# Kernel tuning notes

Hardware: AMD Instinct MI355X
Metric: run time of the kernel (lower is better)

## Reference

```python
import jax, jax.numpy as jnp
import numpy as np

D_MODEL, D_STATE, D_CONV, EXPAND = 32, 64, 4, 2
D_INNER = EXPAND * D_MODEL  # 64 == D_STATE, required by the bmm in the torch source
B, H, W = 4, 48, 48


def setup_inputs() -> dict:
    key = jax.random.key(0)
    ks = jax.random.split(key, 8)
    s = lambda k, sh, sc: jax.random.normal(k, sh, jnp.float32) * sc
    return {
        "x": s(ks[0], (B, H, W, D_MODEL), 1.0),
        "W_in": s(ks[1], (2 * D_INNER, D_MODEL), 0.1),
        "conv_w": s(ks[2], (D_INNER, D_CONV), 0.3),   # depthwise kernel [d_inner, k]
        "conv_b": jnp.zeros((D_INNER,), jnp.float32),
        "W_x": s(ks[3], (D_STATE + 2 * D_INNER, D_INNER), 0.1),
        "W_dt": s(ks[4], (D_INNER, D_STATE), 0.1),
        "b_dt": jnp.zeros((D_INNER,), jnp.float32),
        "A_log": jnp.log(jnp.tile(jnp.arange(1, D_STATE + 1, dtype=jnp.float32), (D_INNER, 1))),
        "D": jnp.ones((D_INNER,), jnp.float32),
        "W_out": s(ks[5], (D_MODEL, D_INNER), 0.1),
    }


def _ssm(x, W_in, conv_w, conv_b, W_x, W_dt, b_dt, A_log, D, W_out):
    # x: [Bn, L, d_model]
    Bn, L, _ = x.shape
    xz = x @ W_in.T                                   # [Bn,L,2*di]
    x_ssm, z = jnp.split(xz, 2, axis=-1)
    # causal depthwise conv1d (pad left k-1, truncate to L)
    xp = jnp.pad(x_ssm, ((0, 0), (D_CONV - 1, 0), (0, 0)))
    xc = conv_b + sum(xp[:, k:k + L, :] * conv_w[:, k] for k in range(D_CONV))
    x_ssm = jax.nn.silu(xc)
    sp = x_ssm @ W_x.T                                # [Bn,L,ds+2*di]
    d_in, Bp, Cp = jnp.split(sp, [D_STATE, D_STATE + D_INNER], axis=-1)
    delta = jax.nn.softplus(d_in @ W_dt.T + b_dt)     # [Bn,L,di]
    A = -jnp.exp(A_log)                               # [di,ds]
    A_bar = jnp.exp(delta[..., None] * A)             # [Bn,L,di,ds]
    B_bar = delta * Bp                                # [Bn,L,di] (broadcast to ds in step)

    def step(h, inp):
        Ab, Bb, c = inp                               # [Bn,di,ds], [Bn,di], [Bn,ds]
        h = Ab * h + Bb[..., None]
        return h, jnp.einsum('bds,bs->bd', h, c)      # == torch.bmm(h, c[...,None])

    h0 = jnp.zeros((Bn, D_INNER, D_STATE), x.dtype)
    _, ys = jax.lax.scan(step, h0, (A_bar.transpose(1, 0, 2, 3),
                                    B_bar.transpose(1, 0, 2),
                                    Cp.transpose(1, 0, 2)))
    y = ys.transpose(1, 0, 2) + D * x_ssm             # skip connection
    y = y * jax.nn.silu(z)                            # gate
    return y @ W_out.T


def reference(x, W_in, conv_w, conv_b, W_x, W_dt, b_dt, A_log, D, W_out):
    p = (W_in, conv_w, conv_b, W_x, W_dt, b_dt, A_log, D, W_out)
    Bsz, Hh, Ww, C = x.shape
    ssm = lambda s: _ssm(s, *p)
    # horizontal scans: sequence along H, batch (b w)
    x_h = x.transpose(0, 2, 1, 3).reshape(Bsz * Ww, Hh, C)
    yh_f = ssm(x_h)
    yh_b = ssm(x_h[:, ::-1])[:, ::-1]
    back_h = lambda t: t.reshape(Bsz, Ww, Hh, C).transpose(0, 2, 1, 3)
    # vertical scans: sequence along W, batch (b h)
    x_v = x.reshape(Bsz * Hh, Ww, C)
    yv_f = ssm(x_v)
    yv_b = ssm(x_v[:, ::-1])[:, ::-1]
    back_v = lambda t: t.reshape(Bsz, Hh, Ww, C)
    return back_h(yh_f) + back_h(yh_b) + back_v(yv_f) + back_v(yv_b)
```

## Files before the change

kernel.cpp:

```cpp
#include <hip/hip_runtime.h>
#include <hip/hip_bf16.h>


constexpr int BN = 4, SL = 48;
constexpr int NPIX = BN * SL * SL;
constexpr int L = SL;
constexpr int NSEQ = BN * SL;
constexpr int NBLK = 4 * NSEQ;
constexpr int PIXPB = 16;
constexpr int NPWB = NPIX / PIXPB;
constexpr int NPREP = 56;
constexpr int NPREB = NPWB + NPREP;

__global__ __launch_bounds__(256) void k_pre(
    const float* __restrict__ x, const float* __restrict__ Win,
    const float* __restrict__ Wdt, const float* __restrict__ Wx,
    const float* __restrict__ Wout,
    float* __restrict__ xraw, float* __restrict__ slz,
    float* __restrict__ PMs, float* __restrict__ PB,
    float* __restrict__ PC, float* __restrict__ PO,
    float* __restrict__ out) {
  __shared__ float xf[PIXPB * 32];
  __shared__ float wt[32 * 129];
  int bid = blockIdx.x, tid = threadIdx.x;

  for (int e = bid * 256 + tid; e < NPIX * 32; e += NPREB * 256) out[e] = 0.f;

  if (bid < NPWB) {
    int pix0 = bid * PIXPB;
    for (int e = tid; e < PIXPB * 32; e += 256) xf[e] = x[pix0 * 32 + e];
    for (int e = tid; e < 4096; e += 256) {
      int j = e >> 5, k = e & 31;
      wt[k * 129 + j] = Win[e];
    }
    __syncthreads();
    int g = tid >> 6, lane = tid & 63;
    float s0[4] = {0.f, 0.f, 0.f, 0.f}, s1[4] = {0.f, 0.f, 0.f, 0.f};
    for (int k = 0; k < 32; ++k) {
      float w0 = wt[k * 129 + lane];
      float w1 = wt[k * 129 + 64 + lane];
      #pragma unroll
      for (int pp = 0; pp < 4; ++pp) {
        float xk = xf[(g * 4 + pp) * 32 + k];
        s0[pp] += w0 * xk;
        s1[pp] += w1 * xk;
      }
    }
    #pragma unroll
    for (int pp = 0; pp < 4; ++pp) {
      int pix = pix0 + g * 4 + pp;
      xraw[pix * 64 + lane] = s0[pp];
      float z = s1[pp];
      slz[pix * 64 + lane] = z / (1.f + __expf(-z));
    }
  } else {
    int e = (bid - NPWB) * 256 + tid;
    if (e < 4096) {
      int i = e >> 6, d = e & 63;
      float s = 0.f;
      #pragma unroll 8
      for (int t = 0; t < 64; ++t) s += Wdt[i * 64 + t] * Wx[t * 64 + d];
      PMs[((d >> 2) * 64 + i) * 4 + (d & 3)] = s;
    } else if (e < 8192) {
      int e2 = e - 4096; int k = e2 >> 6, r = e2 & 63;
      PB[((k >> 2) * 64 + r) * 4 + (k & 3)] = Wx[(64 + r) * 64 + k];
    } else if (e < 12288) {
      int e2 = e - 8192; int k = e2 >> 6, r = e2 & 63;
      PC[((k >> 2) * 64 + r) * 4 + (k & 3)] = Wx[(128 + r) * 64 + k];
    } else {
      int e2 = e - 12288; int c = e2 & 31, d = e2 >> 5;
      PO[((d >> 2) * 32 + c) * 4 + (d & 3)] = Wout[c * 64 + d];
    }
  }
}

__global__ __launch_bounds__(256) void k_scan(
    const float* __restrict__ xraw, const float* __restrict__ slz,
    const float* __restrict__ PMs, const float* __restrict__ PB,
    const float* __restrict__ PC, const float* __restrict__ PO,
    const float* __restrict__ convw, const float* __restrict__ convb,
    const float* __restrict__ bdt, const float* __restrict__ Alog,
    const float* __restrict__ Dv, float* __restrict__ out) {
  __shared__ float xs_s[L * 64];
  __shared__ float u_s[L * 192];

  int tid = threadIdx.x;
  int bid = blockIdx.x;
  int dir = bid / NSEQ;
  int seq = bid % NSEQ;
  int b = seq / SL, q = seq % SL;
  int pbase, pstride;
  if (dir == 0)      { pbase = (b * SL) * SL + q;           pstride = SL;  }
  else if (dir == 1) { pbase = (b * SL + SL - 1) * SL + q;  pstride = -SL; }
  else if (dir == 2) { pbase = (b * SL + q) * SL;           pstride = 1;   }
  else               { pbase = (b * SL + q) * SL + SL - 1;  pstride = -1;  }

  int wv = tid >> 6, lane = tid & 63;

  float* xr = u_s;
  for (int t = wv; t < L; t += 4)
    xr[t * 64 + lane] = xraw[(pbase + t * pstride) * 64 + lane];
  __syncthreads();

  for (int e = tid; e < L * 64; e += 256) {
    int t = e >> 6, d = e & 63;
    float4 cw = reinterpret_cast<const float4*>(convw)[d];
    float s = convb[d] + xr[t * 64 + d] * cw.w;
    if (t >= 1) s += xr[(t - 1) * 64 + d] * cw.z;
    if (t >= 2) s += xr[(t - 2) * 64 + d] * cw.y;
    if (t >= 3) s += xr[(t - 3) * 64 + d] * cw.x;
    xs_s[e] = s / (1.f + __expf(-s));
  }
  __syncthreads();

  {
    int tr = wv * 12;
    float aD[12], aB[12], aC[12];
    #pragma unroll
    for (int j = 0; j < 12; ++j) { aD[j] = 0.f; aB[j] = 0.f; aC[j] = 0.f; }
    const float4* pms = reinterpret_cast<const float4*>(PMs);
    const float4* pb  = reinterpret_cast<const float4*>(PB);
    const float4* pc  = reinterpret_cast<const float4*>(PC);
    for (int k4 = 0; k4 < 16; ++k4) {
      float4 wd = pms[k4 * 64 + lane];
      float4 wb = pb[k4 * 64 + lane];
      float4 wc = pc[k4 * 64 + lane];
      #pragma unroll
      for (int j = 0; j < 12; ++j) {
        float4 x4 = *reinterpret_cast<const float4*>(xs_s + (tr + j) * 64 + k4 * 4);
        aD[j] += wd.x * x4.x + wd.y * x4.y + wd.z * x4.z + wd.w * x4.w;
        aB[j] += wb.x * x4.x + wb.y * x4.y + wb.z * x4.z + wb.w * x4.w;
        aC[j] += wc.x * x4.x + wc.y * x4.y + wc.z * x4.z + wc.w * x4.w;
      }
    }
    float bdl = bdt[lane];
    #pragma unroll
    for (int j = 0; j < 12; ++j) {
      float s = aD[j] + bdl;
      s = (s > 15.f) ? s : __logf(1.f + __expf(s));
      u_s[(tr + j) * 192 + lane]       = s;
      u_s[(tr + j) * 192 + 64 + lane]  = aB[j];
      u_s[(tr + j) * 192 + 128 + lane] = aC[j];
    }
  }
  __syncthreads();

  {
    int d = tid >> 2, sg = tid & 3;
    float A_[16], h[16];
    #pragma unroll
    for (int j = 0; j < 16; ++j) {
      A_[j] = -__expf(Alog[d * 64 + sg * 16 + j]);
      h[j] = 0.f;
    }
    float Dd = Dv[d];
    for (int t = 0; t < L; ++t) {
      float dlt = u_s[t * 192 + d];
      float bb  = dlt * u_s[t * 192 + 64 + d];
      const float* cp = u_s + t * 192 + 128 + sg * 16;
      float part = 0.f;
      #pragma unroll
      for (int j = 0; j < 16; ++j) {
        float ab = __expf(dlt * A_[j]);
        h[j] = ab * h[j] + bb;
        part += h[j] * cp[j];
      }
      part += __shfl_xor(part, 1);
      part += __shfl_xor(part, 2);
      if (sg == 0) u_s[t * 192 + d] = part + Dd * xs_s[t * 64 + d];
    }
  }
  __syncthreads();

  for (int e = tid; e < L * 64; e += 256) {
    int t = e >> 6, d = e & 63;
    u_s[t * 192 + d] *= slz[(pbase + t * pstride) * 64 + d];
  }
  __syncthreads();

  for (int e = tid; e < L * 32; e += 256) {
    int t = e >> 5, c = e & 31;
    const float4* po = reinterpret_cast<const float4*>(PO);
    const float* yv = u_s + t * 192;
    float s = 0.f;
    #pragma unroll
    for (int d4 = 0; d4 < 16; ++d4) {
      float4 w = po[d4 * 32 + c];
      const float* yp = yv + d4 * 4;
      s += w.x * yp[0] + w.y * yp[1] + w.z * yp[2] + w.w * yp[3];
    }
    atomicAdd(&out[(pbase + t * pstride) * 32 + c], s);
  }
}

extern "C" void kernel_launch(void* const* d_in, const int* in_sizes, int n_in,
                              void* d_out, int out_size, void* d_ws, size_t ws_size,
                              hipStream_t stream) {
  const float* x     = (const float*)d_in[0];
  const float* Win   = (const float*)d_in[1];
  const float* convw = (const float*)d_in[2];
  const float* convb = (const float*)d_in[3];
  const float* Wx    = (const float*)d_in[4];
  const float* Wdt   = (const float*)d_in[5];
  const float* bdt   = (const float*)d_in[6];
  const float* Alog  = (const float*)d_in[7];
  const float* Dv    = (const float*)d_in[8];
  const float* Wout  = (const float*)d_in[9];

  float* xraw = (float*)d_ws;
  float* slz  = xraw + NPIX * 64;
  float* PMs  = slz + NPIX * 64;
  float* PB   = PMs + 4096;
  float* PC   = PB + 4096;
  float* PO   = PC + 4096;
  float* out  = (float*)d_out;

  k_pre<<<NPREB, 256, 0, stream>>>(x, Win, Wdt, Wx, Wout, xraw, slz,
                                   PMs, PB, PC, PO, out);
  k_scan<<<NBLK, 256, 0, stream>>>(xraw, slz, PMs, PB, PC, PO, convw, convb,
                                   bdt, Alog, Dv, out);
}
```

Before: 135.9 us.

## Use bf16 MFMA for B/C projections and geometric A_bar recurrence in scan

Moves the B and C projections (x_ssm @ W_x rows 64..191) from scalar fp32 FMAs onto bf16 MFMA 16x16x32 instructions. It packs the weights into fragment layout in the prep kernel and stores a swizzled bf16 copy of x_ssm in shared memory. The scan detects at runtime when A is an arithmetic progression per row and builds the 16 exp(delta*A) values from two exp2 calls plus multiplies, instead of 16 exps. Shared memory is reorganised into smaller bf16 buffers, and launch bounds request 4 blocks per CU. B and C are stored in bf16, which lowers precision in the recurrence.

New measurement: 124.2 us. 8.6% less time.

```diff
diff --git a/kernel.cpp b/kernel.cpp
--- a/kernel.cpp
+++ b/kernel.cpp
@@ -1,5 +1,6 @@
 #include <hip/hip_runtime.h>
 #include <hip/hip_bf16.h>
+#include <stdint.h>
 
 
 constexpr int BN = 4, SL = 48;
@@ -12,14 +13,23 @@
 constexpr int NPREP = 56;
 constexpr int NPREB = NPWB + NPREP;
 
+typedef __attribute__((ext_vector_type(8))) short short8;
+typedef __attribute__((ext_vector_type(4))) float f32x4;
+
+#define DEVINL __device__ __forceinline__
+DEVINL ushort f2b(float f) {
+  uint u = __float_as_uint(f);
+  return (ushort)((u + 0x7FFFu + ((u >> 16) & 1u)) >> 16);
+}
+DEVINL float b2f(ushort u) { return __uint_as_float(((uint)u) << 16); }
+
 __global__ __launch_bounds__(256) void k_pre(
     const float* __restrict__ x, const float* __restrict__ Win,
     const float* __restrict__ Wdt, const float* __restrict__ Wx,
     const float* __restrict__ Wout,
     float* __restrict__ xraw, float* __restrict__ slz,
-    float* __restrict__ PMs, float* __restrict__ PB,
-    float* __restrict__ PC, float* __restrict__ PO,
-    float* __restrict__ out) {
+    float* __restrict__ PMs, float* __restrict__ PO,
+    ushort* __restrict__ PW2, float* __restrict__ out) {
   __shared__ float xf[PIXPB * 32];
   __shared__ float wt[32 * 129];
   int bid = blockIdx.x, tid = threadIdx.x;
@@ -61,12 +71,12 @@
       #pragma unroll 8
       for (int t = 0; t < 64; ++t) s += Wdt[i * 64 + t] * Wx[t * 64 + d];
       PMs[((d >> 2) * 64 + i) * 4 + (d & 3)] = s;
-    } else if (e < 8192) {
-      int e2 = e - 4096; int k = e2 >> 6, r = e2 & 63;
-      PB[((k >> 2) * 64 + r) * 4 + (k & 3)] = Wx[(64 + r) * 64 + k];
     } else if (e < 12288) {
-      int e2 = e - 8192; int k = e2 >> 6, r = e2 & 63;
-      PC[((k >> 2) * 64 + r) * 4 + (k & 3)] = Wx[(128 + r) * 64 + k];
+      int e2 = e - 4096;
+      int j = e2 & 7, l = (e2 >> 3) & 63, ks = (e2 >> 9) & 1, nt = e2 >> 10;
+      int k = ks * 32 + ((l >> 4) * 8) + j;
+      int row = 64 + nt * 16 + (l & 15);
+      PW2[e2] = f2b(Wx[row * 64 + k]);
     } else {
       int e2 = e - 12288; int c = e2 & 31, d = e2 >> 5;
       PO[((d >> 2) * 32 + c) * 4 + (d & 3)] = Wout[c * 64 + d];
@@ -74,15 +84,17 @@
   }
 }
 
-__global__ __launch_bounds__(256) void k_scan(
+__global__ __launch_bounds__(256, 4) void k_scan(
     const float* __restrict__ xraw, const float* __restrict__ slz,
-    const float* __restrict__ PMs, const float* __restrict__ PB,
-    const float* __restrict__ PC, const float* __restrict__ PO,
+    const float* __restrict__ PMs, const ushort* __restrict__ PW2,
+    const float* __restrict__ PO,
     const float* __restrict__ convw, const float* __restrict__ convb,
     const float* __restrict__ bdt, const float* __restrict__ Alog,
     const float* __restrict__ Dv, float* __restrict__ out) {
-  __shared__ float xs_s[L * 64];
-  __shared__ float u_s[L * 192];
+  __shared__ float R1[L * 64];
+  __shared__ __align__(16) ushort R2u[L * 136];
+  __shared__ float R3[L * 64];
+  __shared__ __align__(16) ushort R4u[L * 64];
 
   int tid = threadIdx.x;
   int bid = blockIdx.x;
@@ -97,40 +109,35 @@
 
   int wv = tid >> 6, lane = tid & 63;
 
-  float* xr = u_s;
   for (int t = wv; t < L; t += 4)
-    xr[t * 64 + lane] = xraw[(pbase + t * pstride) * 64 + lane];
+    R1[t * 64 + lane] = xraw[(pbase + t * pstride) * 64 + lane];
   __syncthreads();
 
   for (int e = tid; e < L * 64; e += 256) {
     int t = e >> 6, d = e & 63;
     float4 cw = reinterpret_cast<const float4*>(convw)[d];
-    float s = convb[d] + xr[t * 64 + d] * cw.w;
-    if (t >= 1) s += xr[(t - 1) * 64 + d] * cw.z;
-    if (t >= 2) s += xr[(t - 2) * 64 + d] * cw.y;
-    if (t >= 3) s += xr[(t - 3) * 64 + d] * cw.x;
-    xs_s[e] = s / (1.f + __expf(-s));
+    float s = convb[d] + R1[t * 64 + d] * cw.w;
+    if (t >= 1) s += R1[(t - 1) * 64 + d] * cw.z;
+    if (t >= 2) s += R1[(t - 2) * 64 + d] * cw.y;
+    if (t >= 3) s += R1[(t - 3) * 64 + d] * cw.x;
+    float xs = s / (1.f + __expf(-s));
+    R3[t * 64 + d] = xs;
+    R4u[t * 64 + (d ^ ((t & 7) << 3))] = f2b(xs);
   }
   __syncthreads();
 
   {
     int tr = wv * 12;
-    float aD[12], aB[12], aC[12];
-    #pragma unroll
-    for (int j = 0; j < 12; ++j) { aD[j] = 0.f; aB[j] = 0.f; aC[j] = 0.f; }
+    float aD[12];
+    #pragma unroll
+    for (int j = 0; j < 12; ++j) aD[j] = 0.f;
     const float4* pms = reinterpret_cast<const float4*>(PMs);
-    const float4* pb  = reinterpret_cast<const float4*>(PB);
-    const float4* pc  = reinterpret_cast<const float4*>(PC);
     for (int k4 = 0; k4 < 16; ++k4) {
       float4 wd = pms[k4 * 64 + lane];
-      float4 wb = pb[k4 * 64 + lane];
-      float4 wc = pc[k4 * 64 + lane];
       #pragma unroll
       for (int j = 0; j < 12; ++j) {
-        float4 x4 = *reinterpret_cast<const float4*>(xs_s + (tr + j) * 64 + k4 * 4);
+        float4 x4 = *reinterpret_cast<const float4*>(&R3[(tr + j) * 64 + k4 * 4]);
         aD[j] += wd.x * x4.x + wd.y * x4.y + wd.z * x4.z + wd.w * x4.w;
-        aB[j] += wb.x * x4.x + wb.y * x4.y + wb.z * x4.z + wb.w * x4.w;
-        aC[j] += wc.x * x4.x + wc.y * x4.y + wc.z * x4.z + wc.w * x4.w;
       }
     }
     float bdl = bdt[lane];
@@ -138,50 +145,116 @@
     for (int j = 0; j < 12; ++j) {
       float s = aD[j] + bdl;
       s = (s > 15.f) ? s : __logf(1.f + __expf(s));
-      u_s[(tr + j) * 192 + lane]       = s;
-      u_s[(tr + j) * 192 + 64 + lane]  = aB[j];
-      u_s[(tr + j) * 192 + 128 + lane] = aC[j];
-    }
+      R1[(tr + j) * 64 + lane] = s;
+    }
+  }
+
+  {
+    short8 bfrag[2][2];
+    const short8* pw8 = reinterpret_cast<const short8*>(PW2);
+    #pragma unroll
+    for (int ntl = 0; ntl < 2; ++ntl)
+      #pragma unroll
+      for (int ks = 0; ks < 2; ++ks)
+        bfrag[ntl][ks] = pw8[((2 * wv + ntl) * 2 + ks) * 64 + lane];
+    f32x4 acc[3][2];
+    #pragma unroll
+    for (int mt = 0; mt < 3; ++mt)
+      #pragma unroll
+      for (int ntl = 0; ntl < 2; ++ntl)
+        acc[mt][ntl] = (f32x4){0.f, 0.f, 0.f, 0.f};
+    #pragma unroll
+    for (int mt = 0; mt < 3; ++mt) {
+      int row = mt * 16 + (lane & 15);
+      #pragma unroll
+      for (int ks = 0; ks < 2; ++ks) {
+        int within = (ks * 32 + ((lane >> 4) * 8)) ^ ((row & 7) << 3);
+        short8 af = *reinterpret_cast<const short8*>(&R4u[row * 64 + within]);
+        acc[mt][0] = __builtin_amdgcn_mfma_f32_16x16x32_bf16(af, bfrag[0][ks], acc[mt][0], 0, 0, 0);
+        acc[mt][1] = __builtin_amdgcn_mfma_f32_16x16x32_bf16(af, bfrag[1][ks], acc[mt][1], 0, 0, 0);
+      }
+    }
+    #pragma unroll
+    for (int mt = 0; mt < 3; ++mt)
+      #pragma unroll
+      for (int ntl = 0; ntl < 2; ++ntl)
+        #pragma unroll
+        for (int qq = 0; qq < 4; ++qq) {
+          int t = mt * 16 + (lane >> 4) * 4 + qq;
+          int rr = (2 * wv + ntl) * 16 + (lane & 15);
+          R2u[t * 136 + rr] = f2b(acc[mt][ntl][qq]);
+        }
   }
   __syncthreads();
 
   {
     int d = tid >> 2, sg = tid & 3;
-    float A_[16], h[16];
-    #pragma unroll
-    for (int j = 0; j < 16; ++j) {
-      A_[j] = -__expf(Alog[d * 64 + sg * 16 + j]);
-      h[j] = 0.f;
-    }
+    float A_[16];
+    #pragma unroll
+    for (int j = 0; j < 16; ++j) A_[j] = -__expf(Alog[d * 64 + sg * 16 + j]);
+    float a0 = A_[0], dstep = A_[1] - A_[0];
+    bool arith = true;
+    #pragma unroll
+    for (int j = 0; j < 16; ++j)
+      arith = arith && (fabsf(A_[j] - (a0 + j * dstep)) <= 1e-3f * (1.f + fabsf(A_[j])));
+    const float L2E = 1.44269504f;
+    float a0L = a0 * L2E, ddL = dstep * L2E;
+    float A2_[16];
+    #pragma unroll
+    for (int j = 0; j < 16; ++j) A2_[j] = A_[j] * L2E;
+    float h[16];
+    #pragma unroll
+    for (int j = 0; j < 16; ++j) h[j] = 0.f;
     float Dd = Dv[d];
+
     for (int t = 0; t < L; ++t) {
-      float dlt = u_s[t * 192 + d];
-      float bb  = dlt * u_s[t * 192 + 64 + d];
-      const float* cp = u_s + t * 192 + 128 + sg * 16;
+      float dlt = R1[t * 64 + d];
+      float bb = dlt * b2f(R2u[t * 136 + d]);
+      short8 c0 = *reinterpret_cast<const short8*>(&R2u[t * 136 + 64 + sg * 16]);
+      short8 c1 = *reinterpret_cast<const short8*>(&R2u[t * 136 + 64 + sg * 16 + 8]);
+      float ab[16];
+      if (arith) {
+        float P = exp2f(dlt * a0L);
+        float Rr = exp2f(dlt * ddL);
+        float R2v = Rr * Rr, R4v = R2v * R2v, R8v = R4v * R4v;
+        ab[0] = P;          ab[1] = P * Rr;
+        ab[2] = P * R2v;    ab[3] = ab[1] * R2v;
+        #pragma unroll
+        for (int j = 0; j < 4; ++j) ab[4 + j] = ab[j] * R4v;
+        #pragma unroll
+        for (int j = 0; j < 8; ++j) ab[8 + j] = ab[j] * R8v;
+      } else {
+        #pragma unroll
+        for (int j = 0; j < 16; ++j) ab[j] = exp2f(dlt * A2_[j]);
+      }
       float part = 0.f;
       #pragma unroll
-      for (int j = 0; j < 16; ++j) {
-        float ab = __expf(dlt * A_[j]);
-        h[j] = ab * h[j] + bb;
-        part += h[j] * cp[j];
+      for (int j = 0; j < 8; ++j) {
+        h[j] = ab[j] * h[j] + bb;
+        part += h[j] * b2f((ushort)c0[j]);
+      }
+      #pragma unroll
+      for (int j = 0; j < 8; ++j) {
+        h[8 + j] = ab[8 + j] * h[8 + j] + bb;
+        part += h[8 + j] * b2f((ushort)c1[j]);
       }
       part += __shfl_xor(part, 1);
       part += __shfl_xor(part, 2);
-      if (sg == 0) u_s[t * 192 + d] = part + Dd * xs_s[t * 64 + d];
+      if (sg == 0) R1[t * 64 + d] = part + Dd * R3[t * 64 + d];
     }
   }
   __syncthreads();
 
   for (int e = tid; e < L * 64; e += 256) {
     int t = e >> 6, d = e & 63;
-    u_s[t * 192 + d] *= slz[(pbase + t * pstride) * 64 + d];
+    R1[t * 64 + d] *= slz[(pbase + t * pstride) * 64 + d];
   }
   __syncthreads();
 
   for (int e = tid; e < L * 32; e += 256) {
     int t = e >> 5, c = e & 31;
     const float4* po = reinterpret_cast<const float4*>(PO);
-    const float* yv = u_s + t * 192;
+    const float* yv = R1 + t * 64;
     float s = 0.f;
     #pragma unroll
     for (int d4 = 0; d4 < 16; ++d4) {
@@ -210,13 +283,12 @@
   float* xraw = (float*)d_ws;
   float* slz  = xraw + NPIX * 64;
   float* PMs  = slz + NPIX * 64;
-  float* PB   = PMs + 4096;
-  float* PC   = PB + 4096;
-  float* PO   = PC + 4096;
+  float* PO   = PMs + 4096;
+  ushort* PW2 = (ushort*)(PO + 2048);
   float* out  = (float*)d_out;
 
   k_pre<<<NPREB, 256, 0, stream>>>(x, Win, Wdt, Wx, Wout, xraw, slz,
-                                   PMs, PB, PC, PO, out);
-  k_scan<<<NBLK, 256, 0, stream>>>(xraw, slz, PMs, PB, PC, PO, convw, convb,
+                                   PMs, PO, PW2, out);
+  k_scan<<<NBLK, 256, 0, stream>>>(xraw, slz, PMs, PW2, PO, convw, convb,
                                    bdt, Alog, Dv, out);
 }
```
